# Kernel optimization log

Hardware: AMD Instinct MI355X
Metric: run time of the kernel (lower is better)

## Reference

```python
import jax, jax.numpy as jnp
import numpy as np

COMMITMENT_COST = 1.0


def setup_inputs() -> dict:
    key = jax.random.key(0)
    k1, k2 = jax.random.split(key)
    x = jax.random.normal(k1, (8, 4096, 256), dtype=jnp.float32)
    codebook = jax.random.normal(k2, (2048, 256), dtype=jnp.float32)
    return {"x": x, "codebook": codebook}


def reference(x, codebook):
    # Squared Euclidean distances via the GEMM expansion:
    # argmin over torch.cdist (sqrt is monotone); dist values are unused.
    x2 = jnp.sum(x * x, axis=-1, keepdims=True)            # [B, T, 1]
    c2 = jnp.sum(codebook * codebook, axis=-1)             # [N]
    d2 = x2 - 2.0 * jnp.einsum('btd,nd->btn', x, codebook) + c2  # [B, T, N]
    indices = jnp.argmin(d2, axis=-1)                      # [B, T]
    codes = codebook[indices]                              # [B, T, D]

    code_loss = jnp.mean((codes - jax.lax.stop_gradient(x)) ** 2)
    embedding_loss = jnp.mean((x - jax.lax.stop_gradient(codes)) ** 2) * COMMITMENT_COST
    loss = code_loss + embedding_loss

    # Straight-through estimator
    quantized = x + jax.lax.stop_gradient(codes - x)
    return quantized, indices, loss
```

## Files before the change

kernel.cpp:

```cpp
#include <hip/hip_runtime.h>

#define D   256
#define BM  128
#define BN  128

typedef __attribute__((ext_vector_type(8))) short v8s;
typedef __attribute__((ext_vector_type(4))) float v4f;
#define MFMA16 __builtin_amdgcn_mfma_f32_16x16x32_bf16

#define WAITVM(N) asm volatile("s_waitcnt vmcnt(" #N ")" ::: "memory")
#define SCHEDFENCE() __builtin_amdgcn_sched_barrier(0)

static __device__ inline unsigned short f2bf(float f) {
    unsigned u = __float_as_uint(f);
    return (unsigned short)((u + 0x7fffu + ((u >> 16) & 1u)) >> 16);
}
static __device__ inline float bf2f(unsigned short s) {
    return __uint_as_float(((unsigned)s) << 16);
}

static __device__ inline void gl_lds16(const unsigned short* g, unsigned short* l) {
    __builtin_amdgcn_global_load_lds(
        (const __attribute__((address_space(1))) unsigned int*)g,
        (__attribute__((address_space(3))) unsigned int*)l, 16, 0, 0);
}

__global__ void vq_prep_c2(const float* __restrict__ cb, float* __restrict__ c2,
                           float* __restrict__ loss) {
    const int row  = blockIdx.x;
    const int lane = threadIdx.x;
    if (row == 0 && lane == 0) loss[0] = 0.0f;
    const float4 v = *reinterpret_cast<const float4*>(cb + (size_t)row * D + lane * 4);
    float s = v.x * v.x + v.y * v.y + v.z * v.z + v.w * v.w;
    #pragma unroll
    for (int off = 32; off > 0; off >>= 1) s += __shfl_down(s, off, 64);
    if (lane == 0) c2[row] = s;
}

__global__ void vq_prep_sw(const float* __restrict__ cb,
                           unsigned short* __restrict__ cbh, unsigned short* __restrict__ cbl) {
    const int b     = blockIdx.x;
    const int chunk = b >> 2;
    const int nc = (chunk >> 2) * BN;
    const int kc = (chunk & 3) * 64;
    const int p   = (b & 3) * 256 + threadIdx.x;
    const int seg = p >> 7;
    const int n   = (p & 127) ^ seg;
    const float* src = cb + (size_t)(nc + n) * D + kc + seg * 8;
    const float4 f0 = *reinterpret_cast<const float4*>(src);
    const float4 f1 = *reinterpret_cast<const float4*>(src + 4);
    const float f[8] = {f0.x, f0.y, f0.z, f0.w, f1.x, f1.y, f1.z, f1.w};
    v8s h, l;
    #pragma unroll
    for (int j = 0; j < 8; ++j) {
        unsigned short hb = f2bf(f[j]);
        h[j] = (short)hb;
        l[j] = (short)f2bf(f[j] - bf2f(hb));
    }
    const size_t o = ((size_t)chunk * 1024 + p) * 8;
    *reinterpret_cast<v8s*>(cbh + o) = h;
    *reinterpret_cast<v8s*>(cbl + o) = l;
}

__global__ __launch_bounds__(512, 2) void vq_argmin_mfma(
        const float* __restrict__ x, const float* __restrict__ cb,
        const unsigned short* __restrict__ cbh, const unsigned short* __restrict__ cbl,
        const float* __restrict__ c2, float* __restrict__ idx_out,
        float* __restrict__ qout, float* __restrict__ loss, float scale, int N) {
    __shared__ unsigned short lds_h[2][8192];
    __shared__ unsigned short lds_l[2][8192];
    __shared__ float c2s[2048];

    const int tid  = threadIdx.x;
    const int w    = tid >> 6;
    const int lane = tid & 63;
    const int col  = lane & 15;
    const int quad = lane >> 4;
    const int mg   = w >> 1;
    const int ng   = w & 1;
    const int m0   = blockIdx.x * BM;
    const int n_groups = N >> 7;
    const int n_stages = n_groups * 4;

    const unsigned short* gh0 = cbh + ((size_t)(w * 128 + lane)) * 8;
    const unsigned short* gl0 = cbl + ((size_t)(w * 128 + lane)) * 8;

    gl_lds16(gh0,       &lds_h[0][w * 1024]);
    gl_lds16(gh0 + 512, &lds_h[0][w * 1024 + 512]);
    gl_lds16(gl0,       &lds_l[0][w * 1024]);
    gl_lds16(gl0 + 512, &lds_l[0][w * 1024 + 512]);

    {
        const int o = tid * 8;
        if (o < N) {
            const float4 a = *reinterpret_cast<const float4*>(c2 + o);
            const float4 b = *reinterpret_cast<const float4*>(c2 + o + 4);
            *reinterpret_cast<float4*>(&c2s[o])     = a;
            *reinterpret_cast<float4*>(&c2s[o + 4]) = b;
        }
    }

    v8s xh[2][8], xl[2][8];
    #pragma unroll
    for (int mt = 0; mt < 2; ++mt) {
        const float* xr = x + (size_t)(m0 + mg * 32 + mt * 16 + col) * D;
        #pragma unroll
        for (int ks = 0; ks < 8; ++ks) {
            const int kb = ks * 32 + quad * 8;
            const float4 f0 = *reinterpret_cast<const float4*>(xr + kb);
            const float4 f1 = *reinterpret_cast<const float4*>(xr + kb + 4);
            float f[8] = {f0.x, f0.y, f0.z, f0.w, f1.x, f1.y, f1.z, f1.w};
            v8s h, l;
            #pragma unroll
            for (int j = 0; j < 8; ++j) {
                unsigned short hb = f2bf(f[j]);
                h[j] = (short)hb;
                l[j] = (short)f2bf(f[j] - bf2f(hb));
            }
            xh[mt][ks] = h; xl[mt][ks] = l;
        }
    }

    float runmin[2][4];
    int   runidx[2][4];
    #pragma unroll
    for (int mt = 0; mt < 2; ++mt)
        #pragma unroll
        for (int r = 0; r < 4; ++r) { runmin[mt][r] = 3.4e38f; runidx[mt][r] = 0; }

    v4f acc[4][2];
    #pragma unroll
    for (int nt = 0; nt < 4; ++nt)
        #pragma unroll
        for (int mt = 0; mt < 2; ++mt) acc[nt][mt] = 0.0f;

    __syncthreads();

    for (int g = 0; g < n_groups; ++g) {
        #pragma unroll
        for (int cc = 0; cc < 4; ++cc) {
            const int par   = cc & 1;
            const int stage = g * 4 + cc;
            const bool more = (stage + 1 < n_stages);

            WAITVM(2);
            SCHEDFENCE();
            __builtin_amdgcn_s_barrier();
            SCHEDFENCE();
            if (more) {
                const unsigned short* gh = gh0 + (size_t)(stage + 1) * 8192;
                unsigned short* lh = &lds_h[par ^ 1][w * 1024];
                gl_lds16(gh,       lh);
                gl_lds16(gh + 512, lh + 512);
            }
            __builtin_amdgcn_s_setprio(1);
            #pragma unroll
            for (int ksk = 0; ksk < 2; ++ksk) {
                const int ks  = cc * 2 + ksk;
                const int seg = ksk * 4 + quad;
                #pragma unroll
                for (int nt = 0; nt < 4; ++nt) {
                    const int p = seg * BN + ((ng * 64 + nt * 16 + col) ^ seg);
                    const v8s ch = *reinterpret_cast<const v8s*>(&lds_h[par][p * 8]);
                    #pragma unroll
                    for (int mt = 0; mt < 2; ++mt) {
                        acc[nt][mt] = MFMA16(xh[mt][ks], ch, acc[nt][mt], 0, 0, 0);
                        acc[nt][mt] = MFMA16(xl[mt][ks], ch, acc[nt][mt], 0, 0, 0);
                    }
                }
            }
            __builtin_amdgcn_s_setprio(0);

            if (more) { WAITVM(2); }
            else      { WAITVM(0); }
            SCHEDFENCE();
            __builtin_amdgcn_s_barrier();
            SCHEDFENCE();
            if (more) {
                const unsigned short* gl = gl0 + (size_t)(stage + 1) * 8192;
                unsigned short* ll = &lds_l[par ^ 1][w * 1024];
                gl_lds16(gl,       ll);
                gl_lds16(gl + 512, ll + 512);
            }
            __builtin_amdgcn_s_setprio(1);
            #pragma unroll
            for (int ksk = 0; ksk < 2; ++ksk) {
                const int ks  = cc * 2 + ksk;
                const int seg = ksk * 4 + quad;
                #pragma unroll
                for (int nt = 0; nt < 4; ++nt) {
                    const int p = seg * BN + ((ng * 64 + nt * 16 + col) ^ seg);
                    const v8s cl = *reinterpret_cast<const v8s*>(&lds_l[par][p * 8]);
                    #pragma unroll
                    for (int mt = 0; mt < 2; ++mt)
                        acc[nt][mt] = MFMA16(xh[mt][ks], cl, acc[nt][mt], 0, 0, 0);
                }
            }
            __builtin_amdgcn_s_setprio(0);
        }

        #pragma unroll
        for (int nt = 0; nt < 4; ++nt) {
            const int n = g * BN + ng * 64 + nt * 16 + col;
            const float c2n = c2s[n];
            #pragma unroll
            for (int mt = 0; mt < 2; ++mt) {
                #pragma unroll
                for (int r = 0; r < 4; ++r) {
                    const float s = c2n - 2.0f * acc[nt][mt][r];
                    if (s < runmin[mt][r]) { runmin[mt][r] = s; runidx[mt][r] = n; }
                }
                acc[nt][mt] = 0.0f;
            }
        }
    }

    __syncthreads();
    float* red_v = reinterpret_cast<float*>(&lds_h[0][0]);
    int*   red_i = reinterpret_cast<int*>(&lds_l[0][0]);
    #pragma unroll
    for (int mt = 0; mt < 2; ++mt)
        #pragma unroll
        for (int r = 0; r < 4; ++r) {
            const int row  = mg * 32 + mt * 16 + quad * 4 + r;
            const int slot = (ng * 16 + col) ^ (row & 31);
            red_v[row * 32 + slot] = runmin[mt][r];
            red_i[row * 32 + slot] = runidx[mt][r];
        }
    __syncthreads();
    float best = 3.4e38f;
    int   bidx = 0;
    if (tid < 128) {
        #pragma unroll 4
        for (int t = 0; t < 32; ++t) {
            const int  sl = t ^ (tid & 31);
            const float v = red_v[tid * 32 + sl];
            const int  id = red_i[tid * 32 + sl];
            if (v < best || (v == best && id < bidx)) { best = v; bidx = id; }
        }
        idx_out[m0 + tid] = (float)bidx;
    }
    __syncthreads();
    int* idx_sh = reinterpret_cast<int*>(&lds_h[1][0]);
    if (tid < 128) idx_sh[tid] = bidx;
    __syncthreads();

    const float* xg2 = x + (size_t)m0 * D;
    float s = 0.0f;
    #pragma unroll
    for (int i = 0; i < 16; ++i) {
        const int gix = i * 512 + tid;
        const int row = gix >> 6;
        const int k4  = (gix & 63) * 4;
        const int idx = idx_sh[row];
        const float4 c  = *reinterpret_cast<const float4*>(cb  + (size_t)idx * D + k4);
        const float4 xv = *reinterpret_cast<const float4*>(xg2 + (size_t)row * D + k4);
        *reinterpret_cast<float4*>(qout + (size_t)(m0 + row) * D + k4) = c;
        const float dx = c.x - xv.x, dy = c.y - xv.y, dz = c.z - xv.z, dw = c.w - xv.w;
        s += dx * dx + dy * dy + dz * dz + dw * dw;
    }
    #pragma unroll
    for (int off = 32; off > 0; off >>= 1) s += __shfl_down(s, off, 64);
    float* wsum = reinterpret_cast<float*>(&lds_l[1][0]);
    if ((tid & 63) == 0) wsum[tid >> 6] = s;
    __syncthreads();
    if (tid == 0) {
        float t = 0.0f;
        #pragma unroll
        for (int i = 0; i < 8; ++i) t += wsum[i];
        atomicAdd(loss, t * scale);
    }
}

extern "C" void kernel_launch(void* const* d_in, const int* in_sizes, int n_in,
                              void* d_out, int out_size, void* d_ws, size_t ws_size,
                              hipStream_t stream) {
    const float* x  = (const float*)d_in[0];
    const float* cb = (const float*)d_in[1];
    const int M = in_sizes[0] / D;
    const int N = in_sizes[1] / D;

    float* qout    = (float*)d_out;
    float* idx_out = qout + (size_t)M * D;
    float* loss    = idx_out + M;

    char* wsb = (char*)d_ws;
    float*          c2  = (float*)wsb;
    unsigned short* cbh = (unsigned short*)(wsb + 8192);
    unsigned short* cbl = cbh + (size_t)N * D;

    vq_prep_c2<<<N, 64, 0, stream>>>(cb, c2, loss);
    vq_prep_sw<<<(N / BN) * 4 * 4, 256, 0, stream>>>(cb, cbh, cbl);
    const float scale = 2.0f / (float)((size_t)M * D);
    vq_argmin_mfma<<<M / BM, 512, 0, stream>>>(x, cb, cbh, cbl, c2, idx_out, qout,
                                               loss, scale, N);
}
```

Before: 223.7 us.

## Halve row tile to 64 with 256-thread blocks and merge hi/lo codebook stages

The block shrinks from 128 rows and 512 threads to 64 rows and 256 threads, which doubles the grid to 512 blocks for better CU coverage. The hi and lo codebook copies are now loaded together in one stage behind a single barrier and wait, and each k-step issues three MFMAs, replacing the two half-stages that each had their own barrier. In exchange, each block loads the codebook once for half as many rows, so total codebook traffic doubles. The loads now use vmcnt(0) and no longer keep the earlier partial overlap.

```diff
diff --git a/kernel.cpp b/kernel.cpp
--- a/kernel.cpp
+++ b/kernel.cpp
@@ -1,7 +1,7 @@
 #include <hip/hip_runtime.h>
 
 #define D   256
-#define BM  128
+#define BM  64
 #define BN  128
 
 typedef __attribute__((ext_vector_type(8))) short v8s;
@@ -62,7 +62,7 @@
     *reinterpret_cast<v8s*>(cbl + o) = l;
 }
 
-__global__ __launch_bounds__(512, 2) void vq_argmin_mfma(
+__global__ __launch_bounds__(256, 2) void vq_argmin_mfma(
         const float* __restrict__ x, const float* __restrict__ cb,
         const unsigned short* __restrict__ cbh, const unsigned short* __restrict__ cbl,
         const float* __restrict__ c2, float* __restrict__ idx_out,
@@ -82,13 +82,14 @@
     const int n_groups = N >> 7;
     const int n_stages = n_groups * 4;
 
-    const unsigned short* gh0 = cbh + ((size_t)(w * 128 + lane)) * 8;
-    const unsigned short* gl0 = cbl + ((size_t)(w * 128 + lane)) * 8;
-
-    gl_lds16(gh0,       &lds_h[0][w * 1024]);
-    gl_lds16(gh0 + 512, &lds_h[0][w * 1024 + 512]);
-    gl_lds16(gl0,       &lds_l[0][w * 1024]);
-    gl_lds16(gl0 + 512, &lds_l[0][w * 1024 + 512]);
+    const unsigned short* gh0 = cbh + ((size_t)(w * 256 + lane)) * 8;
+    const unsigned short* gl0 = cbl + ((size_t)(w * 256 + lane)) * 8;
+
+    #pragma unroll
+    for (int i = 0; i < 4; ++i) {
+        gl_lds16(gh0 + i * 512, &lds_h[0][(w * 256 + i * 64) * 8]);
+        gl_lds16(gl0 + i * 512, &lds_l[0][(w * 256 + i * 64) * 8]);
+    }
 
     {
         const int o = tid * 8;
@@ -143,15 +144,21 @@
             const int stage = g * 4 + cc;
             const bool more = (stage + 1 < n_stages);
 
-            WAITVM(2);
+            SCHEDFENCE();
+            WAITVM(0);
             SCHEDFENCE();
             __builtin_amdgcn_s_barrier();
             SCHEDFENCE();
             if (more) {
                 const unsigned short* gh = gh0 + (size_t)(stage + 1) * 8192;
-                unsigned short* lh = &lds_h[par ^ 1][w * 1024];
-                gl_lds16(gh,       lh);
-                gl_lds16(gh + 512, lh + 512);
+                const unsigned short* gl = gl0 + (size_t)(stage + 1) * 8192;
+                unsigned short* lh = &lds_h[par ^ 1][0];
+                unsigned short* ll = &lds_l[par ^ 1][0];
+                #pragma unroll
+                for (int i = 0; i < 4; ++i) {
+                    gl_lds16(gh + i * 512, lh + (w * 256 + i * 64) * 8);
+                    gl_lds16(gl + i * 512, ll + (w * 256 + i * 64) * 8);
+                }
             }
             __builtin_amdgcn_s_setprio(1);
             #pragma unroll
@@ -162,38 +169,13 @@
                 for (int nt = 0; nt < 4; ++nt) {
                     const int p = seg * BN + ((ng * 64 + nt * 16 + col) ^ seg);
                     const v8s ch = *reinterpret_cast<const v8s*>(&lds_h[par][p * 8]);
+                    const v8s cl = *reinterpret_cast<const v8s*>(&lds_l[par][p * 8]);
                     #pragma unroll
                     for (int mt = 0; mt < 2; ++mt) {
                         acc[nt][mt] = MFMA16(xh[mt][ks], ch, acc[nt][mt], 0, 0, 0);
                         acc[nt][mt] = MFMA16(xl[mt][ks], ch, acc[nt][mt], 0, 0, 0);
+                        acc[nt][mt] = MFMA16(xh[mt][ks], cl, acc[nt][mt], 0, 0, 0);
                     }
-                }
-            }
-            __builtin_amdgcn_s_setprio(0);
-
-            if (more) { WAITVM(2); }
-            else      { WAITVM(0); }
-            SCHEDFENCE();
-            __builtin_amdgcn_s_barrier();
-            SCHEDFENCE();
-            if (more) {
-                const unsigned short* gl = gl0 + (size_t)(stage + 1) * 8192;
-                unsigned short* ll = &lds_l[par ^ 1][w * 1024];
-                gl_lds16(gl,       ll);
-                gl_lds16(gl + 512, ll + 512);
-            }
-            __builtin_amdgcn_s_setprio(1);
-            #pragma unroll
-            for (int ksk = 0; ksk < 2; ++ksk) {
-                const int ks  = cc * 2 + ksk;
-                const int seg = ksk * 4 + quad;
-                #pragma unroll
-                for (int nt = 0; nt < 4; ++nt) {
-                    const int p = seg * BN + ((ng * 64 + nt * 16 + col) ^ seg);
-                    const v8s cl = *reinterpret_cast<const v8s*>(&lds_l[par][p * 8]);
-                    #pragma unroll
-                    for (int mt = 0; mt < 2; ++mt)
-                        acc[nt][mt] = MFMA16(xh[mt][ks], cl, acc[nt][mt], 0, 0, 0);
                 }
             }
             __builtin_amdgcn_s_setprio(0);
@@ -230,7 +212,7 @@
     __syncthreads();
     float best = 3.4e38f;
     int   bidx = 0;
-    if (tid < 128) {
+    if (tid < 64) {
         #pragma unroll 4
         for (int t = 0; t < 32; ++t) {
             const int  sl = t ^ (tid & 31);
@@ -242,14 +224,14 @@
     }
     __syncthreads();
     int* idx_sh = reinterpret_cast<int*>(&lds_h[1][0]);
-    if (tid < 128) idx_sh[tid] = bidx;
+    if (tid < 64) idx_sh[tid] = bidx;
     __syncthreads();
 
     const float* xg2 = x + (size_t)m0 * D;
     float s = 0.0f;
     #pragma unroll
     for (int i = 0; i < 16; ++i) {
-        const int gix = i * 512 + tid;
+        const int gix = i * 256 + tid;
         const int row = gix >> 6;
         const int k4  = (gix & 63) * 4;
         const int idx = idx_sh[row];
@@ -265,10 +247,7 @@
     if ((tid & 63) == 0) wsum[tid >> 6] = s;
     __syncthreads();
     if (tid == 0) {
-        float t = 0.0f;
-        #pragma unroll
-        for (int i = 0; i < 8; ++i) t += wsum[i];
-        atomicAdd(loss, t * scale);
+        atomicAdd(loss, (wsum[0] + wsum[1] + wsum[2] + wsum[3]) * scale);
     }
 }
 
@@ -292,6 +271,6 @@
     vq_prep_c2<<<N, 64, 0, stream>>>(cb, c2, loss);
     vq_prep_sw<<<(N / BN) * 4 * 4, 256, 0, stream>>>(cb, cbh, cbl);
     const float scale = 2.0f / (float)((size_t)M * D);
-    vq_argmin_mfma<<<M / BM, 512, 0, stream>>>(x, cb, cbh, cbl, c2, idx_out, qout,
+    vq_argmin_mfma<<<M / BM, 256, 0, stream>>>(x, cb, cbh, cbl, c2, idx_out, qout,
                                                loss, scale, N);
 }
```

Result: faster. 194.5 us (-13.0%).
